# Performance work log

Measured on AMD Instinct MI355X. Metric: run time of the kernel, lower is better.

## Reference

```python
import jax, jax.numpy as jnp
import numpy as np

N = 10000      # nodes
E = 160000     # edges (before self-loops)
H = 4          # heads
C = 256        # per-head channels
D_IN = 512
D_OUT = 512
NEG_SLOPE = 0.2  # PyG GATConv default negative_slope


def gat_conv(x, src, dst, W, a_src, a_dst, bias):
    """PyG-style GATConv with concat=True. x:[n,d_in], W:[d_in,H*C]."""
    n = x.shape[0]
    h = (x @ W).reshape(n, H, C)                       # [n,H,C]
    al_s = jnp.einsum('nhc,hc->nh', h, a_src)          # [n,H]
    al_d = jnp.einsum('nhc,hc->nh', h, a_dst)          # [n,H]
    e = jax.nn.leaky_relu(al_s[src] + al_d[dst], NEG_SLOPE)   # [Etot,H]
    # segment softmax over edges grouped by destination node
    emax = jax.ops.segment_max(e, dst, num_segments=n)
    w = jnp.exp(e - emax[dst])
    denom = jax.ops.segment_sum(w, dst, num_segments=n)
    alpha = w / denom[dst]                             # [Etot,H]
    out = jax.ops.segment_sum(h[src] * alpha[:, :, None], dst, num_segments=n)
    return out.reshape(n, H * C) + bias


def setup_inputs() -> dict:
    key = jax.random.key(0)
    ks = jax.random.split(key, 13)
    s = 0.05
    return {
        'x': jax.random.normal(ks[0], (N, D_IN), jnp.float32),
        'edge_index': jax.random.randint(ks[1], (2, E), 0, N, dtype=jnp.int32),
        'W1': jax.random.normal(ks[2], (D_IN, H * C), jnp.float32) * s,
        'a_src1': jax.random.normal(ks[3], (H, C), jnp.float32) * s,
        'a_dst1': jax.random.normal(ks[4], (H, C), jnp.float32) * s,
        'b1': jnp.zeros((H * C,), jnp.float32),
        'W2': jax.random.normal(ks[5], (H * C, H * C), jnp.float32) * s,
        'a_src2': jax.random.normal(ks[6], (H, C), jnp.float32) * s,
        'a_dst2': jax.random.normal(ks[7], (H, C), jnp.float32) * s,
        'b2': jnp.zeros((H * C,), jnp.float32),
        'Wfc': jax.random.normal(ks[8], (H * C, D_OUT), jnp.float32) * s,
        'bfc': jnp.zeros((D_OUT,), jnp.float32),
    }


def reference(x, edge_index, W1, a_src1, a_dst1, b1, W2, a_src2, a_dst2, b2, Wfc, bfc):
    # PyG GATConv default add_self_loops=True
    loop = jnp.arange(N, dtype=edge_index.dtype)
    src = jnp.concatenate([edge_index[0], loop])
    dst = jnp.concatenate([edge_index[1], loop])
    h = jax.nn.relu(gat_conv(x, src, dst, W1, a_src1, a_dst1, b1))
    # dropout is identity in eval mode
    h = jax.nn.relu(gat_conv(h, src, dst, W2, a_src2, a_dst2, b2))
    return h @ Wfc + bfc
```

## Files before the change

kernel.cpp:

```cpp
#include <hip/hip_runtime.h>

#define NND 10000
#define NED 160000
#define NET 170000
#define MP  10112
#define DH  1024
#define DIN 512
#define DOUT 512
#define SCB 40

typedef unsigned short u16;
typedef __attribute__((ext_vector_type(8))) short short8_t;
typedef __attribute__((ext_vector_type(4))) float f32x4_t;

__device__ __forceinline__ u16 f2bf(float f) {
  unsigned u = __float_as_uint(f);
  return (u16)((u + 0x7fffu + ((u >> 16) & 1u)) >> 16);
}
__device__ __forceinline__ float bf2f(u16 b) {
  return __uint_as_float(((unsigned)b) << 16);
}
__device__ __forceinline__ float bflo(unsigned u) { return __uint_as_float(u << 16); }
__device__ __forceinline__ float bfhi(unsigned u) { return __uint_as_float(u & 0xffff0000u); }
__device__ __forceinline__ float lrelu(float v) { return v > 0.f ? v : 0.2f * v; }

__device__ __forceinline__ void gl_lds16(const void* g, void* l) {
  __builtin_amdgcn_global_load_lds(
      (const __attribute__((address_space(1))) unsigned int*)g,
      (__attribute__((address_space(3))) unsigned int*)l, 16, 0, 0);
}


__global__ void k_prep0(int* __restrict__ indeg,
                        u16* __restrict__ hbp, u16* __restrict__ h2bp) {
  int i = blockIdx.x * 256 + threadIdx.x;
  if (i < NND) indeg[i] = 0;
  const uint4 z = make_uint4(0, 0, 0, 0);
  if (i < (MP - NND) * DH / 8) {
    ((uint4*)hbp)[i] = z;
    ((uint4*)h2bp)[i] = z;
  }
}

__global__ void k_conv_x(const float* __restrict__ x, u16* __restrict__ xb) {
  int i = blockIdx.x * 256 + threadIdx.x;
  const int total = MP * DIN / 4;
  if (i >= total) return;
  float4 v = make_float4(0.f, 0.f, 0.f, 0.f);
  if (i < NND * DIN / 4) v = ((const float4*)x)[i];
  ushort4 o;
  o.x = f2bf(v.x); o.y = f2bf(v.y); o.z = f2bf(v.z); o.w = f2bf(v.w);
  ((ushort4*)xb)[i] = o;
}

__global__ void k_transpose_w(const float* __restrict__ W, u16* __restrict__ WT,
                              int K, int Nt) {
  __shared__ float s[32][33];
  int kt = blockIdx.y * 32, nt = blockIdx.x * 32;
  int tx = threadIdx.x, ty = threadIdx.y;
#pragma unroll
  for (int i = 0; i < 32; i += 8)
    s[ty + i][tx] = W[(size_t)(kt + ty + i) * Nt + nt + tx];
  __syncthreads();
#pragma unroll
  for (int i = 0; i < 32; i += 8)
    WT[(size_t)(nt + ty + i) * K + kt + tx] = f2bf(s[tx][ty + i]);
}


__global__ void k_count(const int* __restrict__ ei, int* __restrict__ indeg) {
  int e = blockIdx.x * 256 + threadIdx.x;
  if (e >= NET) return;
  int dst = (e < NED) ? ei[NED + e] : (e - NED);
  atomicAdd(&indeg[dst], 1);
}

__global__ void k_scan1(const int* __restrict__ indeg, int* __restrict__ rowp,
                        int* __restrict__ bsum) {
  __shared__ int ws[4];
  const int b = blockIdx.x, t = threadIdx.x, wv = t >> 6, ln = t & 63;
  const int i = b * 256 + t;
  int v = (i < NND) ? indeg[i] : 0;
  int sc = v;
#pragma unroll
  for (int off = 1; off < 64; off <<= 1) {
    int xx = __shfl_up(sc, off);
    if (ln >= off) sc += xx;
  }
  if (ln == 63) ws[wv] = sc;
  __syncthreads();
  if (t == 0) {
    int a = 0;
#pragma unroll
    for (int k = 0; k < 4; k++) { int tmp = ws[k]; ws[k] = a; a += tmp; }
    bsum[b] = a;
  }
  __syncthreads();
  sc += ws[wv];
  if (i < NND) rowp[i + 1] = sc;
}

__global__ void k_scan2(int* __restrict__ bsum) {
  int t = threadIdx.x;
  int v = (t < SCB) ? bsum[t] : 0;
  int sc = v;
#pragma unroll
  for (int off = 1; off < 64; off <<= 1) {
    int xx = __shfl_up(sc, off);
    if (t >= off) sc += xx;
  }
  if (t < SCB) bsum[t] = sc - v;
}

__global__ void k_scan3(int* __restrict__ rowp, const int* __restrict__ bsum,
                        int* __restrict__ cursor) {
  const int b = blockIdx.x, t = threadIdx.x;
  const int i = b * 256 + t;
  if (i < NND) { rowp[i + 1] += bsum[b]; cursor[i] = 0; }
  if (i == 0) rowp[0] = 0;
}

__global__ void k_fill(const int* __restrict__ ei, const int* __restrict__ rowp,
                       int* __restrict__ cursor, int* __restrict__ colsrc) {
  int e = blockIdx.x * 256 + threadIdx.x;
  if (e >= NET) return;
  int src, dst;
  if (e < NED) { src = ei[e]; dst = ei[NED + e]; }
  else         { src = dst = e - NED; }
  int pos = rowp[dst] + atomicAdd(&cursor[dst], 1);
  colsrc[pos] = src;
}


template <int KD, int GX, bool HAS_BIAS, bool GUARD, bool OUTBF>
__global__ __launch_bounds__(256) void k_gemm(const u16* __restrict__ A,
                                              const u16* __restrict__ BT,
                                              float* __restrict__ Cf,
                                              u16* __restrict__ Cb,
                                              const float* __restrict__ bias,
                                              int ldc, int mvalid) {
  __shared__ __align__(16) u16 As[128 * 32];
  __shared__ __align__(16) u16 Bs[128 * 32];
  const int tid = threadIdx.x;
  const int lane = tid & 63;
  const int w = tid >> 6;
  const int wr = w >> 1, wc = w & 1;
  const int l15 = lane & 15;
  const int kg = (lane >> 4) * 8;

  const int nwg = GX * gridDim.y;
  const int bid = blockIdx.y * GX + blockIdx.x;
  const int q = nwg >> 3, r = nwg & 7;
  const int xcd = bid & 7, idx = bid >> 3;
  const int swz = (xcd < r ? xcd * (q + 1) : r * (q + 1) + (xcd - r) * q) + idx;
  const int mt = swz / GX, nt = swz % GX;

  const int flat0 = tid * 8;
  const int row0 = flat0 >> 5, kk0 = flat0 & 31;
  const int row1 = 64 + row0;

  const u16* Ab = A + (size_t)(mt * 128) * KD;
  const u16* Bb = BT + (size_t)(nt * 128) * KD;
  const u16* ga0 = Ab + row0 * KD + kk0;
  const u16* ga1 = Ab + row1 * KD + kk0;
  const u16* gb0 = Bb + row0 * KD + kk0;
  const u16* gb1 = Bb + row1 * KD + kk0;
  u16* lA0 = As + flat0;
  u16* lA1 = As + 2048 + flat0;
  u16* lB0 = Bs + flat0;
  u16* lB1 = Bs + 2048 + flat0;

  f32x4_t acc[4][4];
#pragma unroll
  for (int i = 0; i < 4; i++)
#pragma unroll
    for (int j = 0; j < 4; j++)
#pragma unroll
      for (int q2 = 0; q2 < 4; q2++) acc[i][j][q2] = 0.f;

  for (int kt = 0; kt < KD; kt += 32) {
    __syncthreads();
    gl_lds16(ga0 + kt, lA0);
    gl_lds16(ga1 + kt, lA1);
    gl_lds16(gb0 + kt, lB0);
    gl_lds16(gb1 + kt, lB1);
    __syncthreads();
    short8_t af[4], bfr[4];
#pragma unroll
    for (int i = 0; i < 4; i++)
      af[i] = *(const short8_t*)(As + (wr * 64 + i * 16 + l15) * 32 + kg);
#pragma unroll
    for (int i = 0; i < 4; i++)
      bfr[i] = *(const short8_t*)(Bs + (wc * 64 + i * 16 + l15) * 32 + kg);
#pragma unroll
    for (int i = 0; i < 4; i++)
#pragma unroll
      for (int j = 0; j < 4; j++)
        acc[i][j] = __builtin_amdgcn_mfma_f32_16x16x32_bf16(af[i], bfr[j], acc[i][j], 0, 0, 0);
  }

  const int rbase = mt * 128 + wr * 64 + (lane >> 4) * 4;
  const int cbase = nt * 128 + wc * 64 + l15;
#pragma unroll
  for (int i = 0; i < 4; i++) {
#pragma unroll
    for (int j = 0; j < 4; j++) {
#pragma unroll
      for (int q2 = 0; q2 < 4; q2++) {
        int rr = rbase + i * 16 + q2;
        int cc = cbase + j * 16;
        if (!GUARD || rr < mvalid) {
          float v = acc[i][j][q2];
          if (HAS_BIAS) v += bias[cc];
          if (OUTBF) Cb[(size_t)rr * ldc + cc] = f2bf(v);
          else       Cf[(size_t)rr * ldc + cc] = v;
        }
      }
    }
  }
}


__global__ __launch_bounds__(256) void k_al(const u16* __restrict__ hprojb,
                                            const float* __restrict__ a_src,
                                            const float* __restrict__ a_dst,
                                            float* __restrict__ al_s,
                                            float* __restrict__ al_d) {
  int n = blockIdx.x, t = threadIdx.x;
  ushort4 hq = ((const ushort4*)(hprojb + (size_t)n * DH))[t];
  float4 as = ((const float4*)a_src)[t];
  float4 ad = ((const float4*)a_dst)[t];
  float hx = bf2f(hq.x), hy = bf2f(hq.y), hz = bf2f(hq.z), hw = bf2f(hq.w);
  float ps = hx * as.x + hy * as.y + hz * as.z + hw * as.w;
  float pd = hx * ad.x + hy * ad.y + hz * ad.z + hw * ad.w;
#pragma unroll
  for (int off = 32; off; off >>= 1) {
    ps += __shfl_xor(ps, off);
    pd += __shfl_xor(pd, off);
  }
  if ((t & 63) == 0) {
    int h = t >> 6;
    al_s[n * 4 + h] = ps;
    al_d[n * 4 + h] = pd;
  }
}


__global__ __launch_bounds__(64) void k_alpha(const float* __restrict__ al_s,
                                              const float* __restrict__ al_d,
                                              const int* __restrict__ rowp,
                                              const int* __restrict__ colsrc,
                                              float* __restrict__ alpha) {
  const int n = blockIdx.x, ln = threadIdx.x;
  const int beg = rowp[n], end = rowp[n + 1];
  const float4 ad = ((const float4*)al_d)[n];

  float m0 = -1e30f, m1 = -1e30f, m2 = -1e30f, m3 = -1e30f;
  for (int e = beg + ln; e < end; e += 64) {
    int s = colsrc[e];
    float4 as = ((const float4*)al_s)[s];
    m0 = fmaxf(m0, lrelu(as.x + ad.x));
    m1 = fmaxf(m1, lrelu(as.y + ad.y));
    m2 = fmaxf(m2, lrelu(as.z + ad.z));
    m3 = fmaxf(m3, lrelu(as.w + ad.w));
  }
#pragma unroll
  for (int off = 32; off; off >>= 1) {
    m0 = fmaxf(m0, __shfl_xor(m0, off));
    m1 = fmaxf(m1, __shfl_xor(m1, off));
    m2 = fmaxf(m2, __shfl_xor(m2, off));
    m3 = fmaxf(m3, __shfl_xor(m3, off));
  }

  float d0 = 0.f, d1 = 0.f, d2 = 0.f, d3 = 0.f;
  for (int e = beg + ln; e < end; e += 64) {
    int s = colsrc[e];
    float4 as = ((const float4*)al_s)[s];
    float4 wv;
    wv.x = __expf(lrelu(as.x + ad.x) - m0);
    wv.y = __expf(lrelu(as.y + ad.y) - m1);
    wv.z = __expf(lrelu(as.z + ad.z) - m2);
    wv.w = __expf(lrelu(as.w + ad.w) - m3);
    ((float4*)alpha)[e] = wv;
    d0 += wv.x; d1 += wv.y; d2 += wv.z; d3 += wv.w;
  }
#pragma unroll
  for (int off = 32; off; off >>= 1) {
    d0 += __shfl_xor(d0, off);
    d1 += __shfl_xor(d1, off);
    d2 += __shfl_xor(d2, off);
    d3 += __shfl_xor(d3, off);
  }
  const float i0 = 1.f / d0, i1 = 1.f / d1, i2 = 1.f / d2, i3 = 1.f / d3;
  for (int e = beg + ln; e < end; e += 64) {
    float4 wv = ((const float4*)alpha)[e];
    wv.x *= i0; wv.y *= i1; wv.z *= i2; wv.w *= i3;
    ((float4*)alpha)[e] = wv;
  }
}


__global__ __launch_bounds__(64) void k_agg2(const u16* __restrict__ hprojb,
                                             const float* __restrict__ alpha,
                                             const int* __restrict__ rowp,
                                             const int* __restrict__ colsrc,
                                             const float* __restrict__ bias,
                                             u16* __restrict__ outb) {
  const int n = blockIdx.x, half = blockIdx.y, ln = threadIdx.x;
  const int beg = rowp[n], end = rowp[n + 1];
  const int hsel = 2 * half + (ln >> 5);
  const u16* hbase = hprojb + half * 512 + ln * 8;

  float a0 = 0.f, a1 = 0.f, a2 = 0.f, a3 = 0.f;
  float a4 = 0.f, a5 = 0.f, a6 = 0.f, a7 = 0.f;
  int e = beg;
  for (; e + 1 < end; e += 2) {
    int s0 = colsrc[e], s1 = colsrc[e + 1];
    float w0 = alpha[e * 4 + hsel];
    float w1 = alpha[(e + 1) * 4 + hsel];
    uint4 h0 = *(const uint4*)(hbase + (size_t)s0 * DH);
    uint4 h1 = *(const uint4*)(hbase + (size_t)s1 * DH);
    a0 += bflo(h0.x) * w0; a1 += bfhi(h0.x) * w0;
    a2 += bflo(h0.y) * w0; a3 += bfhi(h0.y) * w0;
    a4 += bflo(h0.z) * w0; a5 += bfhi(h0.z) * w0;
    a6 += bflo(h0.w) * w0; a7 += bfhi(h0.w) * w0;
    a0 += bflo(h1.x) * w1; a1 += bfhi(h1.x) * w1;
    a2 += bflo(h1.y) * w1; a3 += bfhi(h1.y) * w1;
    a4 += bflo(h1.z) * w1; a5 += bfhi(h1.z) * w1;
    a6 += bflo(h1.w) * w1; a7 += bfhi(h1.w) * w1;
  }
  if (e < end) {
    int s0 = colsrc[e];
    float w0 = alpha[e * 4 + hsel];
    uint4 h0 = *(const uint4*)(hbase + (size_t)s0 * DH);
    a0 += bflo(h0.x) * w0; a1 += bfhi(h0.x) * w0;
    a2 += bflo(h0.y) * w0; a3 += bfhi(h0.y) * w0;
    a4 += bflo(h0.z) * w0; a5 += bfhi(h0.z) * w0;
    a6 += bflo(h0.w) * w0; a7 += bfhi(h0.w) * w0;
  }

  const float4 bv0 = *(const float4*)(bias + half * 512 + ln * 8);
  const float4 bv1 = *(const float4*)(bias + half * 512 + ln * 8 + 4);
  float o0 = fmaxf(a0 + bv0.x, 0.f), o1 = fmaxf(a1 + bv0.y, 0.f);
  float o2 = fmaxf(a2 + bv0.z, 0.f), o3 = fmaxf(a3 + bv0.w, 0.f);
  float o4 = fmaxf(a4 + bv1.x, 0.f), o5 = fmaxf(a5 + bv1.y, 0.f);
  float o6 = fmaxf(a6 + bv1.z, 0.f), o7 = fmaxf(a7 + bv1.w, 0.f);
  uint4 ob;
  ob.x = (unsigned)f2bf(o0) | ((unsigned)f2bf(o1) << 16);
  ob.y = (unsigned)f2bf(o2) | ((unsigned)f2bf(o3) << 16);
  ob.z = (unsigned)f2bf(o4) | ((unsigned)f2bf(o5) << 16);
  ob.w = (unsigned)f2bf(o6) | ((unsigned)f2bf(o7) << 16);
  *(uint4*)(outb + (size_t)n * DH + half * 512 + ln * 8) = ob;
}


extern "C" void kernel_launch(void* const* d_in, const int* in_sizes, int n_in,
                              void* d_out, int out_size, void* d_ws, size_t ws_size,
                              hipStream_t stream) {
  const float* x   = (const float*)d_in[0];
  const int*   ei  = (const int*)d_in[1];
  const float* W1  = (const float*)d_in[2];
  const float* as1 = (const float*)d_in[3];
  const float* ad1 = (const float*)d_in[4];
  const float* b1  = (const float*)d_in[5];
  const float* W2  = (const float*)d_in[6];
  const float* as2 = (const float*)d_in[7];
  const float* ad2 = (const float*)d_in[8];
  const float* b2  = (const float*)d_in[9];
  const float* Wfc = (const float*)d_in[10];
  const float* bfc = (const float*)d_in[11];
  float* out = (float*)d_out;
  (void)in_sizes; (void)n_in; (void)out_size; (void)ws_size;

  char* p = (char*)d_ws;
  auto carve = [&](size_t bytes) -> char* {
    char* r = p; p += (bytes + 255) & ~(size_t)255; return r;
  };
  u16*   xb     = (u16*)  carve((size_t)MP * DIN * 2);
  u16*   w1t    = (u16*)  carve((size_t)DH * DIN * 2);
  u16*   w2t    = (u16*)  carve((size_t)DH * DH * 2);
  u16*   wft    = (u16*)  carve((size_t)DOUT * DH * 2);
  u16*   hprojb = (u16*)  carve((size_t)MP * DH * 2);
  u16*   hb     = (u16*)  carve((size_t)MP * DH * 2);
  u16*   h2b    = (u16*)  carve((size_t)MP * DH * 2);
  float* als    = (float*)carve((size_t)NND * 4 * 4);
  float* ald    = (float*)carve((size_t)NND * 4 * 4);
  float* alpha  = (float*)carve((size_t)NET * 4 * 4);
  int*   indeg  = (int*)  carve((size_t)NND * 4);
  int*   rowp   = (int*)  carve((size_t)(NND + 1) * 4);
  int*   cursor = (int*)  carve((size_t)NND * 4);
  int*   colsrc = (int*)  carve((size_t)NET * 4);
  int*   bsum   = (int*)  carve((size_t)SCB * 4);

  k_prep0<<<((MP - NND) * DH / 8 + 255) / 256, 256, 0, stream>>>(indeg,
      hb + (size_t)NND * DH, h2b + (size_t)NND * DH);
  k_conv_x<<<(MP * DIN / 4 + 255) / 256, 256, 0, stream>>>(x, xb);
  k_transpose_w<<<dim3(DH / 32, DIN / 32), dim3(32, 8), 0, stream>>>(W1, w1t, DIN, DH);
  k_transpose_w<<<dim3(DH / 32, DH / 32), dim3(32, 8), 0, stream>>>(W2, w2t, DH, DH);
  k_transpose_w<<<dim3(DOUT / 32, DH / 32), dim3(32, 8), 0, stream>>>(Wfc, wft, DH, DOUT);
  k_count<<<(NET + 255) / 256, 256, 0, stream>>>(ei, indeg);
  k_scan1<<<SCB, 256, 0, stream>>>(indeg, rowp, bsum);
  k_scan2<<<1, 64, 0, stream>>>(bsum);
  k_scan3<<<SCB, 256, 0, stream>>>(rowp, bsum, cursor);
  k_fill<<<(NET + 255) / 256, 256, 0, stream>>>(ei, rowp, cursor, colsrc);

  k_gemm<DIN, 8, false, false, true><<<dim3(DH / 128, MP / 128), 256, 0, stream>>>(xb, w1t, nullptr, hprojb, nullptr, DH, MP);
  k_al<<<NND, 256, 0, stream>>>(hprojb, as1, ad1, als, ald);
  k_alpha<<<NND, 64, 0, stream>>>(als, ald, rowp, colsrc, alpha);
  k_agg2<<<dim3(NND, 2), 64, 0, stream>>>(hprojb, alpha, rowp, colsrc, b1, hb);

  k_gemm<DH, 8, false, false, true><<<dim3(DH / 128, MP / 128), 256, 0, stream>>>(hb, w2t, nullptr, hprojb, nullptr, DH, MP);
  k_al<<<NND, 256, 0, stream>>>(hprojb, as2, ad2, als, ald);
  k_alpha<<<NND, 64, 0, stream>>>(als, ald, rowp, colsrc, alpha);
  k_agg2<<<dim3(NND, 2), 64, 0, stream>>>(hprojb, alpha, rowp, colsrc, b2, h2b);

  k_gemm<DH, 4, true, true, false><<<dim3(DOUT / 128, MP / 128), 256, 0, stream>>>(h2b, wft, out, nullptr, bfc, DOUT, NND);
}
```

Measured before the change: 240.6 us.

## Fuse attention logits into GEMM epilogue and softmax into aggregation

Folds the per-node attention dot products into the projection GEMM epilogue, where partial sums are reduced with atomics into zeroed buffers. The separate alpha kernel and its per-edge alpha buffer are removed; aggregation now computes the max, the exp weights and the normalizer on the fly. The prep kernels are merged into one launch. This removes several launches and the round-trips through the edge weights, at the cost of atomics in the GEMM and fp32 logits taken from pre-rounding accumulators.

New measurement: 263.4 us. 1.09x slower.

```diff
diff --git a/kernel.cpp b/kernel.cpp
--- a/kernel.cpp
+++ b/kernel.cpp
@@ -9,6 +9,13 @@
 #define DOUT 512
 #define SCB 40
 
+#define NB_CONV 5056
+#define NB_T1   512
+#define NB_T2   1024
+#define NB_T3   512
+#define NB_Z    80
+#define NB_PREP (NB_CONV + NB_T1 + NB_T2 + NB_T3 + NB_Z)
+
 typedef unsigned short u16;
 typedef __attribute__((ext_vector_type(8))) short short8_t;
 typedef __attribute__((ext_vector_type(4))) float f32x4_t;
@@ -31,33 +38,12 @@
 }
 
 
-__global__ void k_prep0(int* __restrict__ indeg,
-                        u16* __restrict__ hbp, u16* __restrict__ h2bp) {
-  int i = blockIdx.x * 256 + threadIdx.x;
-  if (i < NND) indeg[i] = 0;
-  const uint4 z = make_uint4(0, 0, 0, 0);
-  if (i < (MP - NND) * DH / 8) {
-    ((uint4*)hbp)[i] = z;
-    ((uint4*)h2bp)[i] = z;
-  }
-}
-
-__global__ void k_conv_x(const float* __restrict__ x, u16* __restrict__ xb) {
-  int i = blockIdx.x * 256 + threadIdx.x;
-  const int total = MP * DIN / 4;
-  if (i >= total) return;
-  float4 v = make_float4(0.f, 0.f, 0.f, 0.f);
-  if (i < NND * DIN / 4) v = ((const float4*)x)[i];
-  ushort4 o;
-  o.x = f2bf(v.x); o.y = f2bf(v.y); o.z = f2bf(v.z); o.w = f2bf(v.w);
-  ((ushort4*)xb)[i] = o;
-}
-
-__global__ void k_transpose_w(const float* __restrict__ W, u16* __restrict__ WT,
-                              int K, int Nt) {
+__device__ __forceinline__ void dev_transpose(const float* __restrict__ W,
+                                              u16* __restrict__ WT,
+                                              int K, int Nt, int bx, int by, int t) {
   __shared__ float s[32][33];
-  int kt = blockIdx.y * 32, nt = blockIdx.x * 32;
-  int tx = threadIdx.x, ty = threadIdx.y;
+  const int kt = by * 32, nt = bx * 32;
+  const int tx = t & 31, ty = t >> 5;
 #pragma unroll
   for (int i = 0; i < 32; i += 8)
     s[ty + i][tx] = W[(size_t)(kt + ty + i) * Nt + nt + tx];
@@ -65,6 +51,44 @@
 #pragma unroll
   for (int i = 0; i < 32; i += 8)
     WT[(size_t)(nt + ty + i) * K + kt + tx] = f2bf(s[tx][ty + i]);
+}
+
+__global__ void k_prep(const float* __restrict__ x, u16* __restrict__ xb,
+                       const float* __restrict__ W1, u16* __restrict__ w1t,
+                       const float* __restrict__ W2, u16* __restrict__ w2t,
+                       const float* __restrict__ Wfc, u16* __restrict__ wft,
+                       int* __restrict__ indeg,
+                       u16* __restrict__ hbp, u16* __restrict__ h2bp,
+                       float* __restrict__ als1, float* __restrict__ ald1,
+                       float* __restrict__ als2, float* __restrict__ ald2) {
+  int b = blockIdx.x, t = threadIdx.x;
+  if (b < NB_CONV) {
+    int i = b * 256 + t;
+    float4 v = make_float4(0.f, 0.f, 0.f, 0.f);
+    if (i < NND * DIN / 4) v = ((const float4*)x)[i];
+    ushort4 o;
+    o.x = f2bf(v.x); o.y = f2bf(v.y); o.z = f2bf(v.z); o.w = f2bf(v.w);
+    ((ushort4*)xb)[i] = o;
+    return;
+  }
+  b -= NB_CONV;
+  if (b < NB_T1) { dev_transpose(W1, w1t, DIN, DH, b & 31, b >> 5, t); return; }
+  b -= NB_T1;
+  if (b < NB_T2) { dev_transpose(W2, w2t, DH, DH, b & 31, b >> 5, t); return; }
+  b -= NB_T2;
+  if (b < NB_T3) { dev_transpose(Wfc, wft, DH, DOUT, b & 15, b >> 4, t); return; }
+  b -= NB_T3;
+  {
+    int i = b * 256 + t;
+    const uint4 z = make_uint4(0, 0, 0, 0);
+    if (i < (MP - NND) * DH / 8) { ((uint4*)hbp)[i] = z; ((uint4*)h2bp)[i] = z; }
+    if (i < NND) indeg[i] = 0;
+    if (i < NND) {
+      const float4 zf = make_float4(0.f, 0.f, 0.f, 0.f);
+      ((float4*)als1)[i] = zf; ((float4*)ald1)[i] = zf;
+      ((float4*)als2)[i] = zf; ((float4*)ald2)[i] = zf;
+    }
+  }
 }
 
 
@@ -132,13 +156,17 @@
 }
 
 
-template <int KD, int GX, bool HAS_BIAS, bool GUARD, bool OUTBF>
+template <int KD, int GX, bool HAS_BIAS, bool GUARD, bool OUTBF, bool AL>
 __global__ __launch_bounds__(256) void k_gemm(const u16* __restrict__ A,
                                               const u16* __restrict__ BT,
                                               float* __restrict__ Cf,
                                               u16* __restrict__ Cb,
                                               const float* __restrict__ bias,
-                                              int ldc, int mvalid) {
+                                              int ldc, int mvalid,
+                                              const float* __restrict__ a_src,
+                                              const float* __restrict__ a_dst,
+                                              float* __restrict__ alsum,
+                                              float* __restrict__ aldsum) {
   __shared__ __align__(16) u16 As[128 * 32];
   __shared__ __align__(16) u16 Bs[128 * 32];
   const int tid = threadIdx.x;
@@ -218,90 +246,46 @@
       }
     }
   }
-}
-
-
-__global__ __launch_bounds__(256) void k_al(const u16* __restrict__ hprojb,
-                                            const float* __restrict__ a_src,
-                                            const float* __restrict__ a_dst,
-                                            float* __restrict__ al_s,
-                                            float* __restrict__ al_d) {
-  int n = blockIdx.x, t = threadIdx.x;
-  ushort4 hq = ((const ushort4*)(hprojb + (size_t)n * DH))[t];
-  float4 as = ((const float4*)a_src)[t];
-  float4 ad = ((const float4*)a_dst)[t];
-  float hx = bf2f(hq.x), hy = bf2f(hq.y), hz = bf2f(hq.z), hw = bf2f(hq.w);
-  float ps = hx * as.x + hy * as.y + hz * as.z + hw * as.w;
-  float pd = hx * ad.x + hy * ad.y + hz * ad.z + hw * ad.w;
-#pragma unroll
-  for (int off = 32; off; off >>= 1) {
-    ps += __shfl_xor(ps, off);
-    pd += __shfl_xor(pd, off);
-  }
-  if ((t & 63) == 0) {
-    int h = t >> 6;
-    al_s[n * 4 + h] = ps;
-    al_d[n * 4 + h] = pd;
-  }
-}
-
-
-__global__ __launch_bounds__(64) void k_alpha(const float* __restrict__ al_s,
-                                              const float* __restrict__ al_d,
-                                              const int* __restrict__ rowp,
-                                              const int* __restrict__ colsrc,
-                                              float* __restrict__ alpha) {
-  const int n = blockIdx.x, ln = threadIdx.x;
-  const int beg = rowp[n], end = rowp[n + 1];
-  const float4 ad = ((const float4*)al_d)[n];
-
-  float m0 = -1e30f, m1 = -1e30f, m2 = -1e30f, m3 = -1e30f;
-  for (int e = beg + ln; e < end; e += 64) {
-    int s = colsrc[e];
-    float4 as = ((const float4*)al_s)[s];
-    m0 = fmaxf(m0, lrelu(as.x + ad.x));
-    m1 = fmaxf(m1, lrelu(as.y + ad.y));
-    m2 = fmaxf(m2, lrelu(as.z + ad.z));
-    m3 = fmaxf(m3, lrelu(as.w + ad.w));
-  }
-#pragma unroll
-  for (int off = 32; off; off >>= 1) {
-    m0 = fmaxf(m0, __shfl_xor(m0, off));
-    m1 = fmaxf(m1, __shfl_xor(m1, off));
-    m2 = fmaxf(m2, __shfl_xor(m2, off));
-    m3 = fmaxf(m3, __shfl_xor(m3, off));
-  }
-
-  float d0 = 0.f, d1 = 0.f, d2 = 0.f, d3 = 0.f;
-  for (int e = beg + ln; e < end; e += 64) {
-    int s = colsrc[e];
-    float4 as = ((const float4*)al_s)[s];
-    float4 wv;
-    wv.x = __expf(lrelu(as.x + ad.x) - m0);
-    wv.y = __expf(lrelu(as.y + ad.y) - m1);
-    wv.z = __expf(lrelu(as.z + ad.z) - m2);
-    wv.w = __expf(lrelu(as.w + ad.w) - m3);
-    ((float4*)alpha)[e] = wv;
-    d0 += wv.x; d1 += wv.y; d2 += wv.z; d3 += wv.w;
-  }
-#pragma unroll
-  for (int off = 32; off; off >>= 1) {
-    d0 += __shfl_xor(d0, off);
-    d1 += __shfl_xor(d1, off);
-    d2 += __shfl_xor(d2, off);
-    d3 += __shfl_xor(d3, off);
-  }
-  const float i0 = 1.f / d0, i1 = 1.f / d1, i2 = 1.f / d2, i3 = 1.f / d3;
-  for (int e = beg + ln; e < end; e += 64) {
-    float4 wv = ((const float4*)alpha)[e];
-    wv.x *= i0; wv.y *= i1; wv.z *= i2; wv.w *= i3;
-    ((float4*)alpha)[e] = wv;
+
+  if (AL) {
+    const int head = (nt * 128 + wc * 64) >> 8;
+    float asv[4], adv[4];
+#pragma unroll
+    for (int j = 0; j < 4; j++) {
+      asv[j] = a_src[cbase + j * 16];
+      adv[j] = a_dst[cbase + j * 16];
+    }
+#pragma unroll
+    for (int i = 0; i < 4; i++) {
+#pragma unroll
+      for (int q2 = 0; q2 < 4; q2++) {
+        float ps = 0.f, pd = 0.f;
+#pragma unroll
+        for (int j = 0; j < 4; j++) {
+          ps += acc[i][j][q2] * asv[j];
+          pd += acc[i][j][q2] * adv[j];
+        }
+#pragma unroll
+        for (int off = 8; off; off >>= 1) {
+          ps += __shfl_xor(ps, off);
+          pd += __shfl_xor(pd, off);
+        }
+        if (l15 == 0) {
+          int rr = rbase + i * 16 + q2;
+          if (rr < NND) {
+            atomicAdd(&alsum[rr * 4 + head], ps);
+            atomicAdd(&aldsum[rr * 4 + head], pd);
+          }
+        }
+      }
+    }
   }
 }
 
 
 __global__ __launch_bounds__(64) void k_agg2(const u16* __restrict__ hprojb,
-                                             const float* __restrict__ alpha,
+                                             const float* __restrict__ als,
+                                             const float* __restrict__ ald,
                                              const int* __restrict__ rowp,
                                              const int* __restrict__ colsrc,
                                              const float* __restrict__ bias,
@@ -309,15 +293,23 @@
   const int n = blockIdx.x, half = blockIdx.y, ln = threadIdx.x;
   const int beg = rowp[n], end = rowp[n + 1];
   const int hsel = 2 * half + (ln >> 5);
+  const float adv = ald[n * 4 + hsel];
+
+  float m = -1e30f;
+  for (int e = beg + (ln & 31); e < end; e += 32)
+    m = fmaxf(m, lrelu(als[colsrc[e] * 4 + hsel] + adv));
+#pragma unroll
+  for (int off = 16; off; off >>= 1) m = fmaxf(m, __shfl_xor(m, off));
+
   const u16* hbase = hprojb + half * 512 + ln * 8;
-
   float a0 = 0.f, a1 = 0.f, a2 = 0.f, a3 = 0.f;
   float a4 = 0.f, a5 = 0.f, a6 = 0.f, a7 = 0.f;
+  float ds = 0.f;
   int e = beg;
   for (; e + 1 < end; e += 2) {
     int s0 = colsrc[e], s1 = colsrc[e + 1];
-    float w0 = alpha[e * 4 + hsel];
-    float w1 = alpha[(e + 1) * 4 + hsel];
+    float w0 = __expf(lrelu(als[s0 * 4 + hsel] + adv) - m);
+    float w1 = __expf(lrelu(als[s1 * 4 + hsel] + adv) - m);
     uint4 h0 = *(const uint4*)(hbase + (size_t)s0 * DH);
     uint4 h1 = *(const uint4*)(hbase + (size_t)s1 * DH);
     a0 += bflo(h0.x) * w0; a1 += bfhi(h0.x) * w0;
@@ -328,23 +320,26 @@
     a2 += bflo(h1.y) * w1; a3 += bfhi(h1.y) * w1;
     a4 += bflo(h1.z) * w1; a5 += bfhi(h1.z) * w1;
     a6 += bflo(h1.w) * w1; a7 += bfhi(h1.w) * w1;
+    ds += w0 + w1;
   }
   if (e < end) {
     int s0 = colsrc[e];
-    float w0 = alpha[e * 4 + hsel];
+    float w0 = __expf(lrelu(als[s0 * 4 + hsel] + adv) - m);
     uint4 h0 = *(const uint4*)(hbase + (size_t)s0 * DH);
     a0 += bflo(h0.x) * w0; a1 += bfhi(h0.x) * w0;
     a2 += bflo(h0.y) * w0; a3 += bfhi(h0.y) * w0;
     a4 += bflo(h0.z) * w0; a5 += bfhi(h0.z) * w0;
     a6 += bflo(h0.w) * w0; a7 += bfhi(h0.w) * w0;
-  }
-
+    ds += w0;
+  }
+
+  const float inv = 1.f / ds;
   const float4 bv0 = *(const float4*)(bias + half * 512 + ln * 8);
   const float4 bv1 = *(const float4*)(bias + half * 512 + ln * 8 + 4);
-  float o0 = fmaxf(a0 + bv0.x, 0.f), o1 = fmaxf(a1 + bv0.y, 0.f);
-  float o2 = fmaxf(a2 + bv0.z, 0.f), o3 = fmaxf(a3 + bv0.w, 0.f);
-  float o4 = fmaxf(a4 + bv1.x, 0.f), o5 = fmaxf(a5 + bv1.y, 0.f);
-  float o6 = fmaxf(a6 + bv1.z, 0.f), o7 = fmaxf(a7 + bv1.w, 0.f);
+  float o0 = fmaxf(a0 * inv + bv0.x, 0.f), o1 = fmaxf(a1 * inv + bv0.y, 0.f);
+  float o2 = fmaxf(a2 * inv + bv0.z, 0.f), o3 = fmaxf(a3 * inv + bv0.w, 0.f);
+  float o4 = fmaxf(a4 * inv + bv1.x, 0.f), o5 = fmaxf(a5 * inv + bv1.y, 0.f);
+  float o6 = fmaxf(a6 * inv + bv1.z, 0.f), o7 = fmaxf(a7 * inv + bv1.w, 0.f);
   uint4 ob;
   ob.x = (unsigned)f2bf(o0) | ((unsigned)f2bf(o1) << 16);
   ob.y = (unsigned)f2bf(o2) | ((unsigned)f2bf(o3) << 16);
@@ -383,36 +378,33 @@
   u16*   hprojb = (u16*)  carve((size_t)MP * DH * 2);
   u16*   hb     = (u16*)  carve((size_t)MP * DH * 2);
   u16*   h2b    = (u16*)  carve((size_t)MP * DH * 2);
-  float* als    = (float*)carve((size_t)NND * 4 * 4);
-  float* ald    = (float*)carve((size_t)NND * 4 * 4);
-  float* alpha  = (float*)carve((size_t)NET * 4 * 4);
+  float* als1   = (float*)carve((size_t)NND * 4 * 4);
+  float* ald1   = (float*)carve((size_t)NND * 4 * 4);
+  float* als2   = (float*)carve((size_t)NND * 4 * 4);
+  float* ald2   = (float*)carve((size_t)NND * 4 * 4);
   int*   indeg  = (int*)  carve((size_t)NND * 4);
   int*   rowp   = (int*)  carve((size_t)(NND + 1) * 4);
   int*   cursor = (int*)  carve((size_t)NND * 4);
   int*   colsrc = (int*)  carve((size_t)NET * 4);
   int*   bsum   = (int*)  carve((size_t)SCB * 4);
 
-  k_prep0<<<((MP - NND) * DH / 8 + 255) / 256, 256, 0, stream>>>(indeg,
-      hb + (size_t)NND * DH, h2b + (size_t)NND * DH);
-  k_conv_x<<<(MP * DIN / 4 + 255) / 256, 256, 0, stream>>>(x, xb);
-  k_transpose_w<<<dim3(DH / 32, DIN / 32), dim3(32, 8), 0, stream>>>(W1, w1t, DIN, DH);
-  k_transpose_w<<<dim3(DH / 32, DH / 32), dim3(32, 8), 0, stream>>>(W2, w2t, DH, DH);
-  k_transpose_w<<<dim3(DOUT / 32, DH / 32), dim3(32, 8), 0, stream>>>(Wfc, wft, DH, DOUT);
+  k_prep<<<NB_PREP, 256, 0, stream>>>(x, xb, W1, w1t, W2, w2t, Wfc, wft,
+      indeg, hb + (size_t)NND * DH, h2b + (size_t)NND * DH,
+      als1, ald1, als2, ald2);
   k_count<<<(NET + 255) / 256, 256, 0, stream>>>(ei, indeg);
   k_scan1<<<SCB, 256, 0, stream>>>(indeg, rowp, bsum);
   k_scan2<<<1, 64, 0, stream>>>(bsum);
   k_scan3<<<SCB, 256, 0, stream>>>(rowp, bsum, cursor);
   k_fill<<<(NET + 255) / 256, 256, 0, stream>>>(ei, rowp, cursor, colsrc);
 
-  k_gemm<DIN, 8, false, false, true><<<dim3(DH / 128, MP / 128), 256, 0, stream>>>(xb, w1t, nullptr, hprojb, nullptr, DH, MP);
-  k_al<<<NND, 256, 0, stream>>>(hprojb, as1, ad1, als, ald);
-  k_alpha<<<NND, 64, 0, stream>>>(als, ald, rowp, colsrc, alpha);
-  k_agg2<<<dim3(NND, 2), 64, 0, stream>>>(hprojb, alpha, rowp, colsrc, b1, hb);
-
-  k_gemm<DH, 8, false, false, true><<<dim3(DH / 128, MP / 128), 256, 0, stream>>>(hb, w2t, nullptr, hprojb, nullptr, DH, MP);
-  k_al<<<NND, 256, 0, stream>>>(hprojb, as2, ad2, als, ald);
-  k_alpha<<<NND, 64, 0, stream>>>(als, ald, rowp, colsrc, alpha);
-  k_agg2<<<dim3(NND, 2), 64, 0, stream>>>(hprojb, alpha, rowp, colsrc, b2, h2b);
-
-  k_gemm<DH, 4, true, true, false><<<dim3(DOUT / 128, MP / 128), 256, 0, stream>>>(h2b, wft, out, nullptr, bfc, DOUT, NND);
-}
+  k_gemm<DIN, 8, false, false, true, true><<<dim3(DH / 128, MP / 128), 256, 0, stream>>>(
+      xb, w1t, nullptr, hprojb, nullptr, DH, MP, as1, ad1, als1, ald1);
+  k_agg2<<<dim3(NND, 2), 64, 0, stream>>>(hprojb, als1, ald1, rowp, colsrc, b1, hb);
+
+  k_gemm<DH, 8, false, false, true, true><<<dim3(DH / 128, MP / 128), 256, 0, stream>>>(
+      hb, w2t, nullptr, hprojb, nullptr, DH, MP, as2, ad2, als2, ald2);
+  k_agg2<<<dim3(NND, 2), 64, 0, stream>>>(hprojb, als2, ald2, rowp, colsrc, b2, h2b);
+
+  k_gemm<DH, 4, true, true, false, false><<<dim3(DOUT / 128, MP / 128), 256, 0, stream>>>(
+      h2b, wft, out, nullptr, bfc, DOUT, NND, nullptr, nullptr, nullptr, nullptr);
+}
```
